# Kernel tuning notes

Hardware: AMD Instinct MI355X
Metric: run time of the kernel (lower is better)

The kernel has to match this reference:

```python
import jax, jax.numpy as jnp
import numpy as np


def setup_inputs() -> dict:
    key = jax.random.key(0)
    ks = jax.random.split(key, 8)
    B, C, H, W = 16, 192, 64, 64
    dt_rank, d_state = 12, 1
    return {
        "x": jax.random.normal(ks[0], (B, C, H, W), dtype=jnp.float32),
        "conv_w": jax.random.normal(ks[1], (C, 1, 5, 5), dtype=jnp.float32) * 0.1,
        "conv_b": jax.random.normal(ks[2], (C,), dtype=jnp.float32) * 0.1,
        "x_proj_w": jax.random.normal(ks[3], (dt_rank + 2 * d_state, C), dtype=jnp.float32) * (C ** -0.5),
        "dt_w": jax.random.normal(ks[4], (C, dt_rank), dtype=jnp.float32) * (dt_rank ** -0.5),
        "dt_b": jax.random.normal(ks[5], (C,), dtype=jnp.float32) * 0.1,
        "A_logs": jnp.zeros((C, d_state), dtype=jnp.float32),  # log(arange(1,d_state+1)) with d_state=1 -> 0
        "Ds": jnp.ones((C,), dtype=jnp.float32),
    }


def reference(x, conv_w, conv_b, x_proj_w, dt_w, dt_b, A_logs, Ds):
    B, C, H, W = x.shape
    L = H * W
    dt_rank = dt_w.shape[1]
    n = A_logs.shape[1]  # d_state
    # depthwise conv2d, kernel 5, padding SAME (=d_conv//2), then SiLU
    x = jax.lax.conv_general_dilated(
        x, conv_w, window_strides=(1, 1), padding='SAME',
        feature_group_count=C, dimension_numbers=('NCHW', 'OIHW', 'NCHW'))
    x = jax.nn.silu(x + conv_b[None, :, None, None])
    xs = x.reshape(B, C, L)  # (b, d, l)
    # x_proj: (dt_rank + 2n, C) @ (b, C, l)
    x_dbl = jnp.einsum('kc,bcl->bkl', x_proj_w, xs)
    dts, Bs, Cs = jnp.split(x_dbl, [dt_rank, dt_rank + n], axis=1)
    # dt projection + softplus (delta_softplus=True with delta_bias)
    delta = jax.nn.softplus(jnp.einsum('cr,brl->bcl', dt_w, dts) + dt_b[None, :, None])  # (b,d,l)
    A = -jnp.exp(A_logs)  # (d, n)
    # selective scan returning the full state trajectory h_t (b,d,n,l):
    # h_t = exp(delta_t * A) * h_{t-1} + delta_t * B_t * u_t
    a = jnp.exp(delta[:, :, None, :] * A[None, :, :, None])        # (b,d,n,l)
    b_el = delta[:, :, None, :] * Bs[:, None, :, :] * xs[:, :, None, :]  # (b,d,n,l)

    def combine(e1, e2):
        a1, b1 = e1
        a2, b2 = e2
        return (a1 * a2, a2 * b1 + b2)

    _, h = jax.lax.associative_scan(combine, (a, b_el), axis=-1)  # h: (b,d,n,l)
    state = h.reshape(B, C * n, L)
    # y = C_t * h_t + D * u (fp32, d_state=1 broadcast)
    y = state.astype(jnp.float32) * Cs.astype(jnp.float32) + xs * Ds[:, None]
    return y.reshape(B, C, H, W)
```

## Files before the change

kernel.cpp:

```cpp
#include <hip/hip_runtime.h>
#include <hip/hip_bf16.h>
#include <cstddef>

#define BB 16
#define CC 192
#define HH 64
#define WW 64
#define LL 4096
#define DTR 12
#define KK 14

__device__ __forceinline__ float silu_f(float v) {
  return v / (1.f + __expf(-v));
}

__global__ __launch_bounds__(256, 4) void conv_silu_kernel(
    const float* __restrict__ x, const float* __restrict__ cw,
    const float* __restrict__ cb, float* __restrict__ xs) {
  const int bc = blockIdx.x;
  const int c = bc % CC;
  const int tid = threadIdx.x;
  const int lane = tid & 63;
  const int wv = tid >> 6;
  const int oy0 = wv * 16;

  float w[25];
#pragma unroll
  for (int k = 0; k < 25; ++k) w[k] = cw[c * 25 + k];
  const float bias = cb[c];

  const float* xp = x + (size_t)bc * LL + lane;
  float* op = xs + (size_t)bc * LL + lane;

  float rv[20];
#pragma unroll
  for (int r = 0; r < 20; ++r) {
    const int gr = oy0 + r - 2;
    float v = 0.f;
    if ((unsigned)gr < 64u) v = xp[gr * 64];
    rv[r] = v;
  }

  float acc[5];
#pragma unroll
  for (int i = 0; i < 5; ++i) acc[i] = 0.f;

#pragma unroll
  for (int r = 0; r < 20; ++r) {
    float v = rv[r];
    float vm2 = __shfl_up(v, 2u, 64);
    float vm1 = __shfl_up(v, 1u, 64);
    float vp1 = __shfl_down(v, 1u, 64);
    float vp2 = __shfl_down(v, 2u, 64);
    if (lane < 2) vm2 = 0.f;
    if (lane < 1) vm1 = 0.f;
    if (lane > 62) vp1 = 0.f;
    if (lane > 61) vp2 = 0.f;
    float t[5] = {vm2, vm1, v, vp1, vp2};
#pragma unroll
    for (int ky = 0; ky < 5; ++ky) {
      if (r >= ky && (r - ky) < 16) {
        float s = acc[(r - ky) % 5];
#pragma unroll
        for (int kx = 0; kx < 5; ++kx) s += w[ky * 5 + kx] * t[kx];
        acc[(r - ky) % 5] = s;
      }
    }
    if (r >= 4) {
      const int yf = oy0 + r - 4;
      float a = acc[(r - 4) % 5] + bias;
      op[yf * 64] = silu_f(a);
      acc[(r - 4) % 5] = 0.f;
    }
  }
}

__global__ __launch_bounds__(512, 4) void proj_kernel(
    const float* __restrict__ xs, const float* __restrict__ xpw,
    float* __restrict__ xdbl) {
  const int b = blockIdx.y;
  const int l0 = blockIdx.x * 128;
  const int tid = threadIdx.x;
  const int lane = tid & 63;
  const int g = tid >> 6;

  __shared__ float part[8][KK][132];

  float2 acc[KK];
#pragma unroll
  for (int k = 0; k < KK; ++k) acc[k] = make_float2(0.f, 0.f);

  const float* bp = xs + ((size_t)(b * CC + g * 24)) * LL + l0 + lane * 2;
#pragma unroll 4
  for (int cc = 0; cc < 24; ++cc) {
    float2 v = *(const float2*)(bp + (size_t)cc * LL);
    const int c = g * 24 + cc;
#pragma unroll
    for (int k = 0; k < KK; ++k) {
      float wv = xpw[k * CC + c];
      acc[k].x += wv * v.x;
      acc[k].y += wv * v.y;
    }
  }
#pragma unroll
  for (int k = 0; k < KK; ++k)
    *(float2*)&part[g][k][lane * 2] = acc[k];
  __syncthreads();

  for (int idx = tid; idx < KK * 128; idx += 512) {
    int k = idx >> 7, ln = idx & 127;
    float v = 0.f;
#pragma unroll
    for (int p = 0; p < 8; ++p) v += part[p][k][ln];
    xdbl[((size_t)b * KK + k) * LL + l0 + ln] = v;
  }
}

__global__ __launch_bounds__(1024, 4) void scan_kernel(
    const float* __restrict__ xs, const float* __restrict__ xdbl,
    const float* __restrict__ dtw, const float* __restrict__ dtb,
    const float* __restrict__ A_logs, const float* __restrict__ Ds,
    float* __restrict__ y) {
  const int bc = blockIdx.x;
  const int b = bc / CC;
  const int c = bc - b * CC;
  const int tid = threadIdx.x;
  const int lane = tid & 63;
  const int wv = tid >> 6;

  const float Ac = -__expf(A_logs[c]);
  const float Dc = Ds[c];
  float dw[DTR];
#pragma unroll
  for (int r = 0; r < DTR; ++r) dw[r] = dtw[c * DTR + r];
  const float db = dtb[c];

  const float* xp = xs + (size_t)bc * LL;
  const float* xb = xdbl + (size_t)b * KK * LL;
  float* yp = y + (size_t)bc * LL;

  const int base = wv * 256 + lane * 4;

  float4 x4 = *(const float4*)(xp + base);
  float4 B4 = *(const float4*)(xb + 12 * LL + base);
  float4 C4 = *(const float4*)(xb + 13 * LL + base);
  float4 dr[DTR];
#pragma unroll
  for (int r = 0; r < DTR; ++r)
    dr[r] = *(const float4*)(xb + r * LL + base);

  float xx[4] = {x4.x, x4.y, x4.z, x4.w};
  float bb[4] = {B4.x, B4.y, B4.z, B4.w};
  float av[4], bv[4];
  float aggA = 1.f, aggB = 0.f;
#pragma unroll
  for (int q = 0; q < 4; ++q) {
    float z = db;
#pragma unroll
    for (int r = 0; r < DTR; ++r) z += dw[r] * ((&dr[r].x)[q]);
    float delta = (z > 15.f) ? z : __logf(1.f + __expf(z));
    float a = __expf(delta * Ac);
    float be = delta * bb[q] * xx[q];
    av[q] = a;
    bv[q] = be;
    aggA = a * aggA;
    aggB = a * aggB + be;
  }

  float incA = aggA, incB = aggB;
#pragma unroll
  for (int s = 1; s < 64; s <<= 1) {
    float pA = __shfl_up(incA, (unsigned)s, 64);
    float pB = __shfl_up(incB, (unsigned)s, 64);
    if (lane >= s) {
      incB = incA * pB + incB;
      incA = incA * pA;
    }
  }
  float eA = __shfl_up(incA, 1u, 64);
  float eB = __shfl_up(incB, 1u, 64);
  if (lane == 0) { eA = 1.f; eB = 0.f; }

  __shared__ float wA[16], wB[16];
  if (lane == 63) {
    wA[wv] = incA;
    wB[wv] = incB;
  }
  __syncthreads();

  float pB = 0.f;
  for (int k = 0; k < wv; ++k) pB = wA[k] * pB + wB[k];

  float h = eA * pB + eB;
  float ov[4];
#pragma unroll
  for (int q = 0; q < 4; ++q) {
    h = av[q] * h + bv[q];
    ov[q] = h * ((&C4.x)[q]) + xx[q] * Dc;
  }
  float4 o;
  o.x = ov[0]; o.y = ov[1]; o.z = ov[2]; o.w = ov[3];
  *(float4*)(yp + base) = o;
}

extern "C" void kernel_launch(void* const* d_in, const int* in_sizes, int n_in,
                              void* d_out, int out_size, void* d_ws,
                              size_t ws_size, hipStream_t stream) {
  const float* x        = (const float*)d_in[0];
  const float* conv_w   = (const float*)d_in[1];
  const float* conv_b   = (const float*)d_in[2];
  const float* x_proj_w = (const float*)d_in[3];
  const float* dt_w     = (const float*)d_in[4];
  const float* dt_b     = (const float*)d_in[5];
  const float* A_logs   = (const float*)d_in[6];
  const float* Ds       = (const float*)d_in[7];
  float* out = (float*)d_out;

  char* ws = (char*)d_ws;
  const size_t plane_bytes = (size_t)BB * CC * LL * sizeof(float);
  float* xs   = (float*)ws;
  float* xdbl = (float*)(ws + plane_bytes);

  conv_silu_kernel<<<dim3(BB * CC), 256, 0, stream>>>(x, conv_w, conv_b, xs);
  proj_kernel<<<dim3(LL / 128, BB), 512, 0, stream>>>(xs, x_proj_w, xdbl);
  scan_kernel<<<dim3(BB * CC), 1024, 0, stream>>>(xs, xdbl, dt_w, dt_b,
                                                  A_logs, Ds, out);
}
```

Measured before the change: 180.5 us.

## Store projection output position-major padded to 16 and preload proj inputs

The projection kernel now writes x_dbl as position-major rows of 16 floats (14 values plus padding), so the scan kernel loads all dt/B/C values for a position with contiguous float4 reads instead of 14 separate plane loads. The projection kernel also loads all 24 channel values into registers up front to expose more memory-level parallelism. The padding adds some workspace traffic, and register pressure in the proj kernel increases.

```diff
diff --git a/kernel.cpp b/kernel.cpp
--- a/kernel.cpp
+++ b/kernel.cpp
@@ -9,6 +9,7 @@
 #define LL 4096
 #define DTR 12
 #define KK 14
+#define KP 16
 
 __device__ __forceinline__ float silu_f(float v) {
   return v / (1.f + __expf(-v));
@@ -77,7 +78,7 @@
 
 __global__ __launch_bounds__(512, 4) void proj_kernel(
     const float* __restrict__ xs, const float* __restrict__ xpw,
-    float* __restrict__ xdbl) {
+    float* __restrict__ xdt) {
   const int b = blockIdx.y;
   const int l0 = blockIdx.x * 128;
   const int tid = threadIdx.x;
@@ -86,20 +87,24 @@
 
   __shared__ float part[8][KK][132];
 
+  const float* bp = xs + ((size_t)(b * CC + g * 24)) * LL + l0 + lane * 2;
+  float2 v[24];
+#pragma unroll
+  for (int cc = 0; cc < 24; ++cc)
+    v[cc] = *(const float2*)(bp + (size_t)cc * LL);
+
   float2 acc[KK];
 #pragma unroll
   for (int k = 0; k < KK; ++k) acc[k] = make_float2(0.f, 0.f);
 
-  const float* bp = xs + ((size_t)(b * CC + g * 24)) * LL + l0 + lane * 2;
-#pragma unroll 4
+#pragma unroll
   for (int cc = 0; cc < 24; ++cc) {
-    float2 v = *(const float2*)(bp + (size_t)cc * LL);
     const int c = g * 24 + cc;
 #pragma unroll
     for (int k = 0; k < KK; ++k) {
       float wv = xpw[k * CC + c];
-      acc[k].x += wv * v.x;
-      acc[k].y += wv * v.y;
+      acc[k].x += wv * v[cc].x;
+      acc[k].y += wv * v[cc].y;
     }
   }
 #pragma unroll
@@ -107,17 +112,27 @@
     *(float2*)&part[g][k][lane * 2] = acc[k];
   __syncthreads();
 
-  for (int idx = tid; idx < KK * 128; idx += 512) {
-    int k = idx >> 7, ln = idx & 127;
-    float v = 0.f;
-#pragma unroll
-    for (int p = 0; p < 8; ++p) v += part[p][k][ln];
-    xdbl[((size_t)b * KK + k) * LL + l0 + ln] = v;
+  if (tid < 128) {
+    float val[KP];
+#pragma unroll
+    for (int k = 0; k < KK; ++k) {
+      float s = 0.f;
+#pragma unroll
+      for (int p = 0; p < 8; ++p) s += part[p][k][tid];
+      val[k] = s;
+    }
+    val[14] = 0.f;
+    val[15] = 0.f;
+    float* dst = xdt + ((size_t)b * LL + l0 + tid) * KP;
+#pragma unroll
+    for (int m = 0; m < 4; ++m)
+      *(float4*)(dst + m * 4) = make_float4(val[m * 4], val[m * 4 + 1],
+                                            val[m * 4 + 2], val[m * 4 + 3]);
   }
 }
 
 __global__ __launch_bounds__(1024, 4) void scan_kernel(
-    const float* __restrict__ xs, const float* __restrict__ xdbl,
+    const float* __restrict__ xs, const float* __restrict__ xdt,
     const float* __restrict__ dtw, const float* __restrict__ dtb,
     const float* __restrict__ A_logs, const float* __restrict__ Ds,
     float* __restrict__ y) {
@@ -135,34 +150,31 @@
   for (int r = 0; r < DTR; ++r) dw[r] = dtw[c * DTR + r];
   const float db = dtb[c];
 
-  const float* xp = xs + (size_t)bc * LL;
-  const float* xb = xdbl + (size_t)b * KK * LL;
-  float* yp = y + (size_t)bc * LL;
-
   const int base = wv * 256 + lane * 4;
-
-  float4 x4 = *(const float4*)(xp + base);
-  float4 B4 = *(const float4*)(xb + 12 * LL + base);
-  float4 C4 = *(const float4*)(xb + 13 * LL + base);
-  float4 dr[DTR];
-#pragma unroll
-  for (int r = 0; r < DTR; ++r)
-    dr[r] = *(const float4*)(xb + r * LL + base);
+  const float* xp = xs + (size_t)bc * LL + base;
+  const float* xt = xdt + ((size_t)b * LL + base) * KP;
+  float* yp = y + (size_t)bc * LL + base;
+
+  float4 q[16];
+#pragma unroll
+  for (int i = 0; i < 16; ++i) q[i] = *(const float4*)(xt + i * 4);
+  float4 x4 = *(const float4*)xp;
 
   float xx[4] = {x4.x, x4.y, x4.z, x4.w};
-  float bb[4] = {B4.x, B4.y, B4.z, B4.w};
-  float av[4], bv[4];
+  float av[4], bv[4], cv[4];
   float aggA = 1.f, aggB = 0.f;
 #pragma unroll
-  for (int q = 0; q < 4; ++q) {
+  for (int j = 0; j < 4; ++j) {
+    const float* vals = (const float*)&q[j * 4];
     float z = db;
 #pragma unroll
-    for (int r = 0; r < DTR; ++r) z += dw[r] * ((&dr[r].x)[q]);
+    for (int r = 0; r < DTR; ++r) z += dw[r] * vals[r];
     float delta = (z > 15.f) ? z : __logf(1.f + __expf(z));
     float a = __expf(delta * Ac);
-    float be = delta * bb[q] * xx[q];
-    av[q] = a;
-    bv[q] = be;
+    float be = delta * vals[12] * xx[j];
+    av[j] = a;
+    bv[j] = be;
+    cv[j] = vals[13];
     aggA = a * aggA;
     aggB = a * aggB + be;
   }
@@ -194,13 +206,13 @@
   float h = eA * pB + eB;
   float ov[4];
 #pragma unroll
-  for (int q = 0; q < 4; ++q) {
-    h = av[q] * h + bv[q];
-    ov[q] = h * ((&C4.x)[q]) + xx[q] * Dc;
+  for (int j = 0; j < 4; ++j) {
+    h = av[j] * h + bv[j];
+    ov[j] = h * cv[j] + xx[j] * Dc;
   }
   float4 o;
   o.x = ov[0]; o.y = ov[1]; o.z = ov[2]; o.w = ov[3];
-  *(float4*)(yp + base) = o;
+  *(float4*)yp = o;
 }
 
 extern "C" void kernel_launch(void* const* d_in, const int* in_sizes, int n_in,
@@ -218,11 +230,11 @@
 
   char* ws = (char*)d_ws;
   const size_t plane_bytes = (size_t)BB * CC * LL * sizeof(float);
-  float* xs   = (float*)ws;
-  float* xdbl = (float*)(ws + plane_bytes);
+  float* xs  = (float*)ws;
+  float* xdt = (float*)(ws + plane_bytes);
 
   conv_silu_kernel<<<dim3(BB * CC), 256, 0, stream>>>(x, conv_w, conv_b, xs);
-  proj_kernel<<<dim3(LL / 128, BB), 512, 0, stream>>>(xs, x_proj_w, xdbl);
-  scan_kernel<<<dim3(BB * CC), 1024, 0, stream>>>(xs, xdbl, dt_w, dt_b,
+  proj_kernel<<<dim3(LL / 128, BB), 512, 0, stream>>>(xs, x_proj_w, xdt);
+  scan_kernel<<<dim3(BB * CC), 1024, 0, stream>>>(xs, xdt, dt_w, dt_b,
                                                   A_logs, Ds, out);
 }
```

Measured after the change: 259.0 us. +43.5%, slower.
